# Optimization experiments

Hardware: AMD Instinct MI355X
Metric: run time of the kernel (lower is better)

The kernel has to match this reference:

```python
import jax, jax.numpy as jnp
import numpy as np

H = 32          # num_heads
D = 64          # kv_channels (head dim)
HID = 2048      # hidden_size
MAXPOS = 2048   # max_seq_length


def _rotary_table(num_pos, dim):
    # [num_pos, dim]: sin for first dim/2 cols, cos for last dim/2 cols
    inv_freq = 1.0 / (10000.0 ** (jnp.arange(0, dim, 2, dtype=jnp.float32) / dim))
    t = jnp.arange(num_pos, dtype=jnp.float32)[:, None] * inv_freq[None, :]
    return jnp.concatenate([jnp.sin(t), jnp.cos(t)], axis=1)


def _apply_rope(x, sin, cos):
    # x: [B,S,H,D]; sin,cos: [B,S,D/2]
    sin = jnp.concatenate([sin, sin], axis=-1)[:, :, None, :]  # [B,S,1,D]
    cos = jnp.concatenate([cos, cos], axis=-1)[:, :, None, :]
    half = x.shape[-1] // 2
    x1, x2 = x[..., :half], x[..., half:]
    rot = jnp.concatenate([-x2, x1], axis=-1)
    return x * cos + rot * sin


def setup_inputs() -> dict:
    key = jax.random.key(0)
    k1, k2, k3, k4 = jax.random.split(key, 4)
    B, S = 2, 2048
    hidden_states = jax.random.normal(k1, (B, S, HID), jnp.float32)
    attention_mask = jax.random.randint(k2, (B, 1, S, S), 0, 2).astype(bool)
    position_ids = jnp.broadcast_to(jnp.arange(S, dtype=jnp.int32)[None, :], (B, S))
    W_qkv = jax.random.normal(k3, (3 * H * D, HID), jnp.float32) * 0.02
    W_o = jax.random.normal(k4, (HID, H * D), jnp.float32) * 0.02
    return {"hidden_states": hidden_states, "attention_mask": attention_mask,
            "position_ids": position_ids, "W_qkv": W_qkv, "W_o": W_o}


def reference(hidden_states, attention_mask, position_ids, W_qkv, W_o):
    B, S, _ = hidden_states.shape
    # fused QKV projection (nn.Linear: x @ W.T, no bias)
    qkv = hidden_states @ W_qkv.T                       # [B,S,3*H*D]
    qkv = qkv.reshape(B, S, H, 3 * D)
    q, k, v = jnp.split(qkv, 3, axis=-1)                # each [B,S,H,D]
    sincos = _rotary_table(MAXPOS, D)[position_ids]     # [B,S,D]
    sin, cos = jnp.split(sincos, 2, axis=-1)            # [B,S,D/2] each
    q = _apply_rope(q, sin, cos)
    k = _apply_rope(k, sin, cos)
    scale = jnp.sqrt(jnp.float32(D))
    scores = jnp.einsum('bqhd,bkhd->bhqk', q, k) / scale   # [B,H,S,S]
    scores = jnp.where(attention_mask, jnp.float32(-10000.0), scores)
    weights = jax.nn.softmax(scores, axis=-1)
    attn = jnp.einsum('bhqk,bkhd->bqhd', weights, v)       # [B,S,H,D]
    attn = attn.reshape(B, S, H * D)
    return attn @ W_o.T                                    # [B,S,HID]
```

## Files before the change

kernel.cpp:

```cpp
#include <hip/hip_runtime.h>

#define B_   2
#define S_   2048
#define H_   32
#define D_   64
#define HID_ 2048

typedef unsigned short ushort_t;
typedef __attribute__((ext_vector_type(8))) short short8;
typedef __attribute__((ext_vector_type(4))) float floatx4;

typedef const __attribute__((address_space(1))) char* gas_ptr;
typedef __attribute__((address_space(3))) char* las_ptr;

__device__ __forceinline__ float bf2f(ushort_t u) {
    union { unsigned int i; float f; } v; v.i = ((unsigned int)u) << 16; return v.f;
}
__device__ __forceinline__ ushort_t f2bf(float f) {
    union { float f; unsigned int i; } v; v.f = f;
    unsigned int x = v.i;
    unsigned int r = x + 0x7fffu + ((x >> 16) & 1u);
    return (ushort_t)(r >> 16);
}

__device__ __forceinline__ float fexp2(float x) {
#if __has_builtin(__builtin_amdgcn_exp2f)
    return __builtin_amdgcn_exp2f(x);
#else
    float r; asm("v_exp_f32 %0, %1" : "=v"(r) : "v"(x)); return r;
#endif
}

__device__ __forceinline__ unsigned cvt_pk_bf16(float a, float b) {
    unsigned r;
    asm("v_cvt_pk_bf16_f32 %0, %1, %2" : "=v"(r) : "v"(a), "v"(b));
    return r;
}

__global__ __launch_bounds__(256) void cast_f32_bf16(const float* __restrict__ in,
                                                     ushort_t* __restrict__ out,
                                                     int n8) {
    int i = blockIdx.x * 256 + threadIdx.x;
    if (i >= n8) return;
    const float4* p = (const float4*)(in + (size_t)i * 8);
    float4 a = p[0], b = p[1];
    uint4 o;
    o.x = cvt_pk_bf16(a.x, a.y);
    o.y = cvt_pk_bf16(a.z, a.w);
    o.z = cvt_pk_bf16(b.x, b.y);
    o.w = cvt_pk_bf16(b.z, b.w);
    *(uint4*)(out + (size_t)i * 8) = o;
}

__global__ __launch_bounds__(256) void mask_pack(const int* __restrict__ m,
                                                 unsigned long long* __restrict__ bits) {
    int idx = blockIdx.x * 256 + threadIdx.x;
    unsigned long long bal = __ballot(m[idx] != 0);
    if ((threadIdx.x & 63) == 0) bits[idx >> 6] = bal;
}

__global__ __launch_bounds__(512, 2) void gemm256_bt(const ushort_t* __restrict__ A,
                                                     const ushort_t* __restrict__ Bm,
                                                     ushort_t* __restrict__ C,
                                                     int M, int N, int K) {
    __shared__ ushort_t lA[2][256][64];
    __shared__ ushort_t lB[2][256][64];
    const int tid  = threadIdx.x;
    const int w    = tid >> 6, lane = tid & 63;
    const int quad = lane >> 4, l16 = lane & 15;
    const int wm = w >> 2, wn = w & 3;
    const int sr = lane >> 3, ss = lane & 7;
    const int gseg = (ss ^ sr) * 8;

    const int nbx = N >> 8;
    int id  = blockIdx.x;
    int cpx = gridDim.x >> 3;
    int swz = (id & 7) * cpx + (id >> 3);
    int by = swz / nbx, bx = swz - by * nbx;
    const int m0 = by * 256, n0 = bx * 256;

    int arow[2], brow[2];
    arow[0] = w * 8;                       arow[1] = 128 + w * 8;
    brow[0] = (w >> 2) * 64 + (w & 3) * 8; brow[1] = 128 + brow[0];

    const ushort_t *gAf[2], *gAs[2], *gBf[2], *gBs[2];
#pragma unroll
    for (int c = 0; c < 2; c++) {
        gAf[c] = A  + (size_t)(m0 + arow[c] + sr) * K + gseg;
        gAs[c] = A  + (size_t)(m0 + arow[c] + 64 + sr) * K + gseg;
        gBf[c] = Bm + (size_t)(n0 + brow[c] + sr) * K + gseg;
        gBs[c] = Bm + (size_t)(n0 + brow[c] + 32 + sr) * K + gseg;
    }

#define STAGE_AF(BUF, KT) do { _Pragma("unroll") for (int c = 0; c < 2; c++) \
    __builtin_amdgcn_global_load_lds((gas_ptr)(gAf[c] + (KT)), (las_ptr)&lA[BUF][arow[c]][0], 16, 0, 0); } while (0)
#define STAGE_AS(BUF, KT) do { _Pragma("unroll") for (int c = 0; c < 2; c++) \
    __builtin_amdgcn_global_load_lds((gas_ptr)(gAs[c] + (KT)), (las_ptr)&lA[BUF][arow[c] + 64][0], 16, 0, 0); } while (0)
#define STAGE_BF(BUF, KT) do { _Pragma("unroll") for (int c = 0; c < 2; c++) \
    __builtin_amdgcn_global_load_lds((gas_ptr)(gBf[c] + (KT)), (las_ptr)&lB[BUF][brow[c]][0], 16, 0, 0); } while (0)
#define STAGE_BS(BUF, KT) do { _Pragma("unroll") for (int c = 0; c < 2; c++) \
    __builtin_amdgcn_global_load_lds((gas_ptr)(gBs[c] + (KT)), (las_ptr)&lB[BUF][brow[c] + 32][0], 16, 0, 0); } while (0)

#define LDA_(SUB, BUF) do { _Pragma("unroll") for (int mi = 0; mi < 4; mi++) \
    _Pragma("unroll") for (int ks = 0; ks < 2; ks++) \
        aF[mi][ks] = *(const short8*)&lA[BUF][wm * 128 + (SUB) * 64 + mi * 16 + l16][(((ks * 4 + quad) ^ (l16 & 7)) * 8)]; } while (0)
#define LDB_(SUB, BUF) do { _Pragma("unroll") for (int ni = 0; ni < 2; ni++) \
    _Pragma("unroll") for (int ks = 0; ks < 2; ks++) \
        bF[ni][ks] = *(const short8*)&lB[BUF][wn * 64 + (SUB) * 32 + ni * 16 + l16][(((ks * 4 + quad) ^ (l16 & 7)) * 8)]; } while (0)

#define MM_(Hh, Gg) do { _Pragma("unroll") for (int mi = 0; mi < 4; mi++) \
    _Pragma("unroll") for (int ni = 0; ni < 2; ni++) \
    _Pragma("unroll") for (int ks = 0; ks < 2; ks++) \
        acc[(Hh) * 4 + mi][(Gg) * 2 + ni] = __builtin_amdgcn_mfma_f32_16x16x32_bf16( \
            aF[mi][ks], bF[ni][ks], acc[(Hh) * 4 + mi][(Gg) * 2 + ni], 0, 0, 0); } while (0)

#define VMC6 asm volatile("s_waitcnt vmcnt(6)" ::: "memory")
#define BARR __builtin_amdgcn_s_barrier()
#define SETP1 __builtin_amdgcn_s_setprio(1)
#define SETP0 __builtin_amdgcn_s_setprio(0)

    floatx4 acc[8][4];
#pragma unroll
    for (int i = 0; i < 8; i++)
#pragma unroll
        for (int j = 0; j < 4; j++) acc[i][j] = (floatx4){0.f, 0.f, 0.f, 0.f};
    short8 aF[4][2];
    short8 bF[2][2];

    const int NT = K >> 6;
    const int NI = NT >> 1;

    STAGE_AF(0, 0); STAGE_BF(0, 0); STAGE_AS(0, 0); STAGE_BS(0, 0);
    STAGE_BF(1, 64); STAGE_AS(1, 64); STAGE_BS(1, 64);
    VMC6;
    BARR;

    for (int i = 0; i < NI; ++i) {
        const int t0k = i << 7;
        const int t1k = t0k + 64;
        const int t2k = t0k + 128, t3k = t0k + 192;
        const bool g2 = (t2k < K), g3 = (t3k < K);
        const bool last = (i == NI - 1);

        LDA_(0, 0); LDB_(0, 0);
        STAGE_AF(1, t1k);
        asm volatile("s_waitcnt lgkmcnt(8)" ::: "memory");
        BARR; SETP1; MM_(0, 0); SETP0;
        VMC6; BARR;
        LDA_(1, 0);
        if (g2) STAGE_BF(0, t2k);
        BARR; SETP1; MM_(1, 0); SETP0;
        VMC6; BARR;
        LDB_(1, 0);
        if (g2) STAGE_AS(0, t2k);
        BARR; SETP1; MM_(1, 1); SETP0;
        VMC6; BARR;
        LDA_(0, 0);
        if (g2) STAGE_BS(0, t2k);
        BARR; SETP1; MM_(0, 1); SETP0;
        if (last) { asm volatile("s_waitcnt vmcnt(0)" ::: "memory"); }
        else      { VMC6; }
        BARR;

        LDA_(0, 1); LDB_(0, 1);
        if (g2) STAGE_AF(0, t2k);
        asm volatile("s_waitcnt lgkmcnt(8)" ::: "memory");
        BARR; SETP1; MM_(0, 0); SETP0;
        VMC6; BARR;
        LDA_(1, 1);
        if (g3) STAGE_BF(1, t3k);
        BARR; SETP1; MM_(1, 0); SETP0;
        VMC6; BARR;
        LDB_(1, 1);
        if (g3) STAGE_AS(1, t3k);
        BARR; SETP1; MM_(1, 1); SETP0;
        VMC6; BARR;
        LDA_(0, 1);
        if (g3) STAGE_BS(1, t3k);
        BARR; SETP1; MM_(0, 1); SETP0;
        VMC6; BARR;
    }

#pragma unroll
    for (int mi = 0; mi < 8; mi++)
#pragma unroll
        for (int ni = 0; ni < 4; ni++)
#pragma unroll
            for (int r = 0; r < 4; r++) {
                int row = m0 + wm * 128 + mi * 16 + quad * 4 + r;
                int col = n0 + wn * 64 + ni * 16 + l16;
                C[(size_t)row * N + col] = f2bf(acc[mi][ni][r]);
            }
#undef STAGE_AF
#undef STAGE_AS
#undef STAGE_BF
#undef STAGE_BS
#undef LDA_
#undef LDB_
#undef MM_
#undef VMC6
#undef BARR
#undef SETP1
#undef SETP0
}

template <bool OF32>
__global__ __launch_bounds__(256) void gemm_bt(const ushort_t* __restrict__ A,
                                               const ushort_t* __restrict__ Bm,
                                               void* __restrict__ Cv,
                                               int M, int N, int K) {
    __shared__ ushort_t lA[128 * 32];
    __shared__ ushort_t lB[128 * 32];
    const int tid  = threadIdx.x;
    const int lane = tid & 63, wave = tid >> 6;
    const int quad = lane >> 4, l16 = lane & 15;
    const int wm = wave >> 1, wn = wave & 1;
    const int m0 = blockIdx.y * 128, n0 = blockIdx.x * 128;

    const int srow = tid >> 2;
    const int gseg = (tid & 3) ^ ((tid >> 3) & 3);
    const ushort_t* gA = A + (size_t)(m0 + srow) * K + gseg * 8;
    const ushort_t* gB = Bm + (size_t)(n0 + srow) * K + gseg * 8;

    const int fseg = quad ^ ((l16 >> 1) & 3);

    floatx4 acc[4][4];
#pragma unroll
    for (int i = 0; i < 4; i++)
#pragma unroll
        for (int j = 0; j < 4; j++) acc[i][j] = (floatx4){0.f, 0.f, 0.f, 0.f};

    for (int k0 = 0; k0 < K; k0 += 32) {
#pragma unroll
        for (int j = 0; j < 2; j++) {
            __builtin_amdgcn_global_load_lds(
                (gas_ptr)(gA + (size_t)j * 64 * K + k0),
                (las_ptr)(lA + j * 2048 + wave * 512), 16, 0, 0);
            __builtin_amdgcn_global_load_lds(
                (gas_ptr)(gB + (size_t)j * 64 * K + k0),
                (las_ptr)(lB + j * 2048 + wave * 512), 16, 0, 0);
        }
        __syncthreads();

        short8 aF[4], bF[4];
#pragma unroll
        for (int mi = 0; mi < 4; mi++)
            aF[mi] = *(const short8*)&lA[(wm * 64 + mi * 16 + l16) * 32 + fseg * 8];
#pragma unroll
        for (int ni = 0; ni < 4; ni++)
            bF[ni] = *(const short8*)&lB[(wn * 64 + ni * 16 + l16) * 32 + fseg * 8];
#pragma unroll
        for (int mi = 0; mi < 4; mi++)
#pragma unroll
            for (int ni = 0; ni < 4; ni++)
                acc[mi][ni] = __builtin_amdgcn_mfma_f32_16x16x32_bf16(aF[mi], bF[ni], acc[mi][ni], 0, 0, 0);
        __syncthreads();
    }

#pragma unroll
    for (int mi = 0; mi < 4; mi++)
#pragma unroll
        for (int ni = 0; ni < 4; ni++)
#pragma unroll
            for (int r = 0; r < 4; r++) {
                int row = m0 + wm * 64 + mi * 16 + quad * 4 + r;
                int col = n0 + wn * 64 + ni * 16 + l16;
                if (OF32) ((float*)Cv)[(size_t)row * N + col] = acc[mi][ni][r];
                else      ((ushort_t*)Cv)[(size_t)row * N + col] = f2bf(acc[mi][ni][r]);
            }
}

__global__ __launch_bounds__(256) void rope_qk(const ushort_t* __restrict__ qkv,
                                               const int* __restrict__ pos,
                                               ushort_t* __restrict__ qr,
                                               ushort_t* __restrict__ kr) {
    int idx = blockIdx.x * 256 + threadIdx.x;
    int d = idx & 63;
    int s = (idx >> 6) & 2047;
    int h = (idx >> 17) & 31;
    int b = idx >> 22;
    size_t qbase = ((size_t)(b * S_ + s)) * (3 * H_ * D_) + h * (3 * D_);
    int i  = d & 31;
    int d2 = d ^ 32;
    float x   = bf2f(qkv[qbase + d]);
    float xp  = bf2f(qkv[qbase + d2]);
    float kx  = bf2f(qkv[qbase + 64 + d]);
    float kxp = bf2f(qkv[qbase + 64 + d2]);
    int   p   = pos[b * S_ + s];
    float inv = fexp2((float)i * -0.41524101186092985f);
    float t   = (float)p * inv;
    float c = cosf(t), sn = sinf(t);
    float rq = (d < 32) ? -xp : xp;
    float rk = (d < 32) ? -kxp : kxp;
    float qo = (x * c + rq * sn) * 0.18033688011112042f;
    float ko = kx * c + rk * sn;
    size_t o = ((size_t)(b * H_ + h) * S_ + s) * D_ + d;
    qr[o] = f2bf(qo);
    kr[o] = f2bf(ko);
}

__global__ __launch_bounds__(256) void v_trans(const ushort_t* __restrict__ qkv,
                                               ushort_t* __restrict__ vt) {
    __shared__ ushort_t tile[64][72];
    const int bid = blockIdx.x;
    const int g  = bid >> 5;
    const int s0 = (bid & 31) * 64;
    const int b = g >> 5, h = g & 31;
    const int tid = threadIdx.x;
    const int r = tid >> 2, c = (tid & 3) * 16;
    const ushort_t* src = qkv + ((size_t)(b * S_) + s0 + r) * (3 * H_ * D_) + h * (3 * D_) + 128 + c;
    *(short8*)&tile[r][c]     = *(const short8*)src;
    *(short8*)&tile[r][c + 8] = *(const short8*)(src + 8);
    __syncthreads();
    const int d = tid >> 2, cs = (tid & 3) * 16;
    ushort_t* dst = vt + ((size_t)g * D_ + d) * S_ + s0 + cs;
    short8 o0, o1;
#pragma unroll
    for (int j = 0; j < 8; j++) {
        o0[j] = (short)tile[cs + j][d];
        o1[j] = (short)tile[cs + 8 + j][d];
    }
    *(short8*)dst       = o0;
    *(short8*)(dst + 8) = o1;
}

__global__ __launch_bounds__(256) void attn_kernel(const ushort_t* __restrict__ qr,
                                                   const ushort_t* __restrict__ kr,
                                                   const ushort_t* __restrict__ vt,
                                                   const unsigned long long* __restrict__ mbits,
                                                   ushort_t* __restrict__ ctx) {
    __shared__ ushort_t lK[64 * 64];
    __shared__ ushort_t lV[64 * 64];
    __shared__ ushort_t lds_p[4][16][72];
    const int tid  = threadIdx.x;
    const int wave = tid >> 6, lane = tid & 63;
    const int quad = lane >> 4, l16 = lane & 15;

    const int id   = blockIdx.x;
    const int g    = (id & 7) | ((id >> 8) << 3);
    const int qblk = (id >> 3) & 31;
    const int b    = g >> 5;
    const int q0   = qblk * 64 + wave * 16;
    const size_t headBase = (size_t)g * S_ * D_;
    const unsigned long long* mrow = mbits + ((size_t)b * S_ + q0 + l16) * (S_ / 64);

    const int sr = lane >> 3, ss = lane & 7;
    const int gss = ss ^ sr;
    const ushort_t* gK0 = kr + headBase + (size_t)(wave * 16 + sr) * D_ + gss * 8;
    const ushort_t* gV0 = vt + headBase + (size_t)(wave * 16 + sr) * S_ + gss * 8;

    const int segA0 = ((quad)     ^ (l16 & 7)) * 8;
    const int segA1 = ((quad + 4) ^ (l16 & 7)) * 8;
    const int rowOff = (l16)*64;

    short8 qf0 = *(const short8*)(qr + headBase + (size_t)(q0 + l16) * D_ + quad * 8);
    short8 qf1 = *(const short8*)(qr + headBase + (size_t)(q0 + l16) * D_ + 32 + quad * 8);

    float l_st = 0.f;
    floatx4 o[4];
#pragma unroll
    for (int t = 0; t < 4; t++) o[t] = (floatx4){0.f, 0.f, 0.f, 0.f};

    for (int k0 = 0; k0 < S_; k0 += 64) {
#pragma unroll
        for (int i = 0; i < 2; i++) {
            __builtin_amdgcn_global_load_lds(
                (gas_ptr)(gK0 + (size_t)(k0 + i * 8) * D_),
                (las_ptr)(lK + (wave * 16 + i * 8) * 64), 16, 0, 0);
            __builtin_amdgcn_global_load_lds(
                (gas_ptr)(gV0 + (size_t)(i * 8) * S_ + k0),
                (las_ptr)(lV + (wave * 16 + i * 8) * 64), 16, 0, 0);
        }
        unsigned long long mb = mrow[k0 >> 6];
        __syncthreads();

        floatx4 scT[4];
#pragma unroll
        for (int t = 0; t < 4; t++) scT[t] = (floatx4){0.f, 0.f, 0.f, 0.f};
#pragma unroll
        for (int t = 0; t < 4; t++) {
            short8 kf0 = *(const short8*)&lK[t * 1024 + rowOff + segA0];
            short8 kf1 = *(const short8*)&lK[t * 1024 + rowOff + segA1];
            scT[t] = __builtin_amdgcn_mfma_f32_16x16x32_bf16(kf0, qf0, scT[t], 0, 0, 0);
            scT[t] = __builtin_amdgcn_mfma_f32_16x16x32_bf16(kf1, qf1, scT[t], 0, 0, 0);
        }

        unsigned mlo = (unsigned)(mb >> (quad * 4));
        unsigned mhi = (unsigned)(mb >> (quad * 4 + 32));
        float pv[4][4];
        float rs = 0.f;
#pragma unroll
        for (int t = 0; t < 4; t++) {
            unsigned msrc = (t < 2) ? mlo : mhi;
#pragma unroll
            for (int r = 0; r < 4; r++) {
                int bitpos = (t & 1) * 16 + r;
                float e = fexp2(scT[t][r]);
                e = ((msrc >> bitpos) & 1u) ? 0.f : e;
                pv[t][r] = e;
                rs += e;
            }
        }
        l_st += rs;

#pragma unroll
        for (int t = 0; t < 4; t++) {
            uint2 w;
            w.x = cvt_pk_bf16(pv[t][0], pv[t][1]);
            w.y = cvt_pk_bf16(pv[t][2], pv[t][3]);
            *(uint2*)&lds_p[wave][l16][t * 16 + quad * 4] = w;
        }
        short8 pf0 = *(const short8*)&lds_p[wave][l16][quad * 8];
        short8 pf1 = *(const short8*)&lds_p[wave][l16][32 + quad * 8];

#pragma unroll
        for (int t = 0; t < 4; t++) {
            short8 vf0 = *(const short8*)&lV[t * 1024 + rowOff + segA0];
            short8 vf1 = *(const short8*)&lV[t * 1024 + rowOff + segA1];
            o[t] = __builtin_amdgcn_mfma_f32_16x16x32_bf16(pf0, vf0, o[t], 0, 0, 0);
            o[t] = __builtin_amdgcn_mfma_f32_16x16x32_bf16(pf1, vf1, o[t], 0, 0, 0);
        }
        __syncthreads();
    }

    l_st += __shfl_xor(l_st, 16);
    l_st += __shfl_xor(l_st, 32);
    float li[4];
#pragma unroll
    for (int r = 0; r < 4; r++) li[r] = 1.0f / __shfl(l_st, quad * 4 + r, 16);
#pragma unroll
    for (int t = 0; t < 4; t++)
#pragma unroll
        for (int r = 0; r < 4; r++) {
            int srow = q0 + quad * 4 + r;
            ctx[((size_t)(b * S_) + srow) * (H_ * D_) + (g & 31) * D_ + t * 16 + l16] = f2bf(o[t][r] * li[r]);
        }
}

extern "C" void kernel_launch(void* const* d_in, const int* in_sizes, int n_in,
                              void* d_out, int out_size, void* d_ws, size_t ws_size,
                              hipStream_t stream) {
    const float* hidden          = (const float*)d_in[0];
    const int* mask              = (const int*)d_in[1];
    const int* pos               = (const int*)d_in[2];
    const float* Wqkv            = (const float*)d_in[3];
    const float* Wo              = (const float*)d_in[4];
    float* out                   = (float*)d_out;

    char* ws = (char*)d_ws;
    ushort_t* qkv     = (ushort_t*)(ws);
    ushort_t* ctx     = (ushort_t*)(ws);
    unsigned long long* mbits = (unsigned long long*)(ws + 16777216);
    ushort_t* Wo_bf   = (ushort_t*)(ws + 50331648);
    ushort_t* hid_bf  = (ushort_t*)(ws + 58720256);
    ushort_t* Wqkv_bf = (ushort_t*)(ws + 75497472);
    ushort_t* q_r     = (ushort_t*)(ws + 58720256);
    ushort_t* k_r     = (ushort_t*)(ws + 75497472);
    ushort_t* v_t     = (ushort_t*)(ws + 92274688);

    {
        int n8 = (B_ * S_ * HID_) / 8;
        cast_f32_bf16<<<n8 / 256, 256, 0, stream>>>(hidden, hid_bf, n8);
        n8 = (3 * H_ * D_ * HID_) / 8;
        cast_f32_bf16<<<n8 / 256, 256, 0, stream>>>(Wqkv, Wqkv_bf, n8);
        n8 = (HID_ * H_ * D_) / 8;
        cast_f32_bf16<<<n8 / 256, 256, 0, stream>>>(Wo, Wo_bf, n8);
    }

    gemm256_bt<<<((3 * H_ * D_) / 256) * ((B_ * S_) / 256), 512, 0, stream>>>(
        hid_bf, Wqkv_bf, qkv, B_ * S_, 3 * H_ * D_, HID_);

    int nElem = B_ * H_ * S_ * D_;
    rope_qk<<<nElem / 256, 256, 0, stream>>>(qkv, pos, q_r, k_r);
    v_trans<<<B_ * H_ * (S_ / 64), 256, 0, stream>>>(qkv, v_t);

    mask_pack<<<(B_ * S_ * S_) / 256, 256, 0, stream>>>(mask, mbits);

    attn_kernel<<<2048, 256, 0, stream>>>(q_r, k_r, v_t, mbits, ctx);

    gemm_bt<true><<<dim3(HID_ / 128, (B_ * S_) / 128), 256, 0, stream>>>(
        ctx, Wo_bf, out, B_ * S_, HID_, H_ * D_);
}
```

Measured before the change: 363.2 us.

## Restructure 256x256 GEMM main loop into per-tile ping-pong with double B fragments

Rewrites the big GEMM's K-loop from a two-tile unrolled schedule into a per-64-K-tile loop with a two-iteration epilogue. It double-buffers the B register fragments (bF0/bF1) and reorders the MMA quadrants so that each LDS fragment load is issued right after an MFMA block, with sched_barrier fences keeping the compiler from moving them. The aim is to overlap LDS reads and global-to-LDS staging with MFMA work and to drop the per-iteration guard branches. In exchange it uses more VGPRs and relies on a hand-tuned vmcnt wait sequence in the tail, which could cause races or register spills if any count is wrong.

```diff
diff --git a/kernel.cpp b/kernel.cpp
--- a/kernel.cpp
+++ b/kernel.cpp
@@ -104,20 +104,24 @@
 #define LDA_(SUB, BUF) do { _Pragma("unroll") for (int mi = 0; mi < 4; mi++) \
     _Pragma("unroll") for (int ks = 0; ks < 2; ks++) \
         aF[mi][ks] = *(const short8*)&lA[BUF][wm * 128 + (SUB) * 64 + mi * 16 + l16][(((ks * 4 + quad) ^ (l16 & 7)) * 8)]; } while (0)
-#define LDB_(SUB, BUF) do { _Pragma("unroll") for (int ni = 0; ni < 2; ni++) \
+#define LDB_(SUB, BUF, BV) do { _Pragma("unroll") for (int ni = 0; ni < 2; ni++) \
     _Pragma("unroll") for (int ks = 0; ks < 2; ks++) \
-        bF[ni][ks] = *(const short8*)&lB[BUF][wn * 64 + (SUB) * 32 + ni * 16 + l16][(((ks * 4 + quad) ^ (l16 & 7)) * 8)]; } while (0)
-
-#define MM_(Hh, Gg) do { _Pragma("unroll") for (int mi = 0; mi < 4; mi++) \
+        BV[ni][ks] = *(const short8*)&lB[BUF][wn * 64 + (SUB) * 32 + ni * 16 + l16][(((ks * 4 + quad) ^ (l16 & 7)) * 8)]; } while (0)
+
+#define MM_(Hh, Gg, BV) do { _Pragma("unroll") for (int mi = 0; mi < 4; mi++) \
     _Pragma("unroll") for (int ni = 0; ni < 2; ni++) \
     _Pragma("unroll") for (int ks = 0; ks < 2; ks++) \
         acc[(Hh) * 4 + mi][(Gg) * 2 + ni] = __builtin_amdgcn_mfma_f32_16x16x32_bf16( \
-            aF[mi][ks], bF[ni][ks], acc[(Hh) * 4 + mi][(Gg) * 2 + ni], 0, 0, 0); } while (0)
+            aF[mi][ks], BV[ni][ks], acc[(Hh) * 4 + mi][(Gg) * 2 + ni], 0, 0, 0); } while (0)
 
 #define VMC6 asm volatile("s_waitcnt vmcnt(6)" ::: "memory")
+#define VMC4 asm volatile("s_waitcnt vmcnt(4)" ::: "memory")
+#define VMC2 asm volatile("s_waitcnt vmcnt(2)" ::: "memory")
+#define VMC0 asm volatile("s_waitcnt vmcnt(0)" ::: "memory")
 #define BARR __builtin_amdgcn_s_barrier()
 #define SETP1 __builtin_amdgcn_s_setprio(1)
 #define SETP0 __builtin_amdgcn_s_setprio(0)
+#define SCHED0 __builtin_amdgcn_sched_barrier(0)
 
     floatx4 acc[8][4];
 #pragma unroll
@@ -125,60 +129,84 @@
 #pragma unroll
         for (int j = 0; j < 4; j++) acc[i][j] = (floatx4){0.f, 0.f, 0.f, 0.f};
     short8 aF[4][2];
-    short8 bF[2][2];
+    short8 bF0[2][2];
+    short8 bF1[2][2];
 
     const int NT = K >> 6;
-    const int NI = NT >> 1;
-
-    STAGE_AF(0, 0); STAGE_BF(0, 0); STAGE_AS(0, 0); STAGE_BS(0, 0);
-    STAGE_BF(1, 64); STAGE_AS(1, 64); STAGE_BS(1, 64);
+
+    STAGE_AF(0, 0); STAGE_BF(0, 0); STAGE_BS(0, 0); STAGE_AS(0, 0);
+    STAGE_AF(1, 64); STAGE_BF(1, 64);
     VMC6;
     BARR;
-
-    for (int i = 0; i < NI; ++i) {
-        const int t0k = i << 7;
-        const int t1k = t0k + 64;
-        const int t2k = t0k + 128, t3k = t0k + 192;
-        const bool g2 = (t2k < K), g3 = (t3k < K);
-        const bool last = (i == NI - 1);
-
-        LDA_(0, 0); LDB_(0, 0);
-        STAGE_AF(1, t1k);
-        asm volatile("s_waitcnt lgkmcnt(8)" ::: "memory");
-        BARR; SETP1; MM_(0, 0); SETP0;
+    LDA_(0, 0);
+    LDB_(0, 0, bF0);
+
+    for (int t = 0; t < NT - 2; ++t) {
+        const int buf = t & 1, nb = buf ^ 1;
+        const int kt1 = (t + 1) << 6, kt2 = (t + 2) << 6;
+
+        STAGE_BS(nb, kt1);
+        BARR; SETP1; MM_(0, 0, bF0); SETP0;
+        SCHED0;
+        LDB_(1, buf, bF1);
         VMC6; BARR;
-        LDA_(1, 0);
-        if (g2) STAGE_BF(0, t2k);
-        BARR; SETP1; MM_(1, 0); SETP0;
+
+        STAGE_AS(nb, kt1);
+        BARR; SETP1; MM_(0, 1, bF1); SETP0;
+        SCHED0;
+        LDA_(1, buf);
         VMC6; BARR;
-        LDB_(1, 0);
-        if (g2) STAGE_AS(0, t2k);
-        BARR; SETP1; MM_(1, 1); SETP0;
+
+        STAGE_AF(buf, kt2);
+        BARR; SETP1; MM_(1, 1, bF1); SETP0;
         VMC6; BARR;
-        LDA_(0, 0);
-        if (g2) STAGE_BS(0, t2k);
-        BARR; SETP1; MM_(0, 1); SETP0;
-        if (last) { asm volatile("s_waitcnt vmcnt(0)" ::: "memory"); }
-        else      { VMC6; }
+
+        STAGE_BF(buf, kt2);
+        BARR; SETP1; MM_(1, 0, bF0); SETP0;
+        SCHED0;
+        LDA_(0, nb);
+        LDB_(0, nb, bF0);
+        VMC6; BARR;
+    }
+
+    {
+        const int t = NT - 2;
+        const int buf = t & 1, nb = buf ^ 1;
+        const int kt1 = (t + 1) << 6;
+
+        STAGE_BS(nb, kt1);
+        BARR; SETP1; MM_(0, 0, bF0); SETP0;
+        SCHED0; LDB_(1, buf, bF1);
+        VMC6; BARR;
+
+        STAGE_AS(nb, kt1);
+        BARR; SETP1; MM_(0, 1, bF1); SETP0;
+        SCHED0; LDA_(1, buf);
+        VMC6; BARR;
+
+        BARR; SETP1; MM_(1, 1, bF1); SETP0;
+        VMC4; BARR;
+
+        BARR; SETP1; MM_(1, 0, bF0); SETP0;
+        SCHED0; LDA_(0, nb); LDB_(0, nb, bF0);
+        VMC2; BARR;
+    }
+
+    {
+        const int buf = (NT - 1) & 1;
+
+        BARR; SETP1; MM_(0, 0, bF0); SETP0;
+        SCHED0; LDB_(1, buf, bF1);
+        VMC0; BARR;
+
+        BARR; SETP1; MM_(0, 1, bF1); SETP0;
+        SCHED0; LDA_(1, buf);
         BARR;
 
-        LDA_(0, 1); LDB_(0, 1);
-        if (g2) STAGE_AF(0, t2k);
-        asm volatile("s_waitcnt lgkmcnt(8)" ::: "memory");
-        BARR; SETP1; MM_(0, 0); SETP0;
-        VMC6; BARR;
-        LDA_(1, 1);
-        if (g3) STAGE_BF(1, t3k);
-        BARR; SETP1; MM_(1, 0); SETP0;
-        VMC6; BARR;
-        LDB_(1, 1);
-        if (g3) STAGE_AS(1, t3k);
-        BARR; SETP1; MM_(1, 1); SETP0;
-        VMC6; BARR;
-        LDA_(0, 1);
-        if (g3) STAGE_BS(1, t3k);
-        BARR; SETP1; MM_(0, 1); SETP0;
-        VMC6; BARR;
+        BARR; SETP1; MM_(1, 1, bF1); SETP0;
+        BARR;
+
+        BARR; SETP1; MM_(1, 0, bF0); SETP0;
     }
 
 #pragma unroll
@@ -199,9 +227,13 @@
 #undef LDB_
 #undef MM_
 #undef VMC6
+#undef VMC4
+#undef VMC2
+#undef VMC0
 #undef BARR
 #undef SETP1
 #undef SETP0
+#undef SCHED0
 }
 
 template <bool OF32>
```

Measured after the change: 365.4 us. About the same (+0.6%).

## Prefetch next K/V tile in attention and widen output-projection GEMM tiles

Applied to the files above, without the earlier changes.

The attention loop now loads all K and V fragments from LDS into registers right after the barrier, syncs, and then issues the global-to-LDS copy for the next tile. That copy overlaps with the QK^T, softmax and PV compute instead of being exposed at the start of every iteration. The output projection GEMM moves to 512-thread blocks with 128x256 tiles and grouped block-index swizzling, which improves operand reuse and L2 locality. In exchange, register pressure rises because the kf/vf arrays are held across the compute, and the wider GEMM launches fewer blocks.

```diff
diff --git a/kernel.cpp b/kernel.cpp
--- a/kernel.cpp
+++ b/kernel.cpp
@@ -136,9 +136,8 @@
     BARR;
 
     for (int i = 0; i < NI; ++i) {
-        const int t0k = i << 7;
-        const int t1k = t0k + 64;
-        const int t2k = t0k + 128, t3k = t0k + 192;
+        const int t1k = (i << 7) + 64;
+        const int t2k = t1k + 64, t3k = t1k + 128;
         const bool g2 = (t2k < K), g3 = (t3k < K);
         const bool last = (i == NI - 1);
 
@@ -205,24 +204,32 @@
 }
 
 template <bool OF32>
-__global__ __launch_bounds__(256) void gemm_bt(const ushort_t* __restrict__ A,
-                                               const ushort_t* __restrict__ Bm,
-                                               void* __restrict__ Cv,
-                                               int M, int N, int K) {
-    __shared__ ushort_t lA[128 * 32];
-    __shared__ ushort_t lB[128 * 32];
+__global__ __launch_bounds__(512, 4) void gemm_wide_bt(const ushort_t* __restrict__ A,
+                                                       const ushort_t* __restrict__ Bm,
+                                                       void* __restrict__ Cv,
+                                                       int M, int N, int K) {
+    __shared__ ushort_t lA[128][32];
+    __shared__ ushort_t lB[256][32];
     const int tid  = threadIdx.x;
-    const int lane = tid & 63, wave = tid >> 6;
+    const int w    = tid >> 6, lane = tid & 63;
     const int quad = lane >> 4, l16 = lane & 15;
-    const int wm = wave >> 1, wn = wave & 1;
-    const int m0 = blockIdx.y * 128, n0 = blockIdx.x * 128;
-
-    const int srow = tid >> 2;
-    const int gseg = (tid & 3) ^ ((tid >> 3) & 3);
-    const ushort_t* gA = A + (size_t)(m0 + srow) * K + gseg * 8;
-    const ushort_t* gB = Bm + (size_t)(n0 + srow) * K + gseg * 8;
-
-    const int fseg = quad ^ ((l16 >> 1) & 3);
+    const int wm = w >> 2, wn = w & 3;
+
+    const int sr = lane >> 2, ss = lane & 3;
+    const int gss = ss ^ ((sr >> 1) & 3);
+
+    const int nbx = N >> 8;
+    int id  = blockIdx.x;
+    int cpx = gridDim.x >> 3;
+    int swz = (id & 7) * cpx + (id >> 3);
+    int by = swz / nbx, bx = swz - by * nbx;
+    const int m0 = by * 128, n0 = bx * 256;
+
+    const ushort_t* gA  = A  + (size_t)(m0 + w * 16 + sr) * K + gss * 8;
+    const ushort_t* gB0 = Bm + (size_t)(n0 + w * 32 + sr) * K + gss * 8;
+    const ushort_t* gB1 = gB0 + (size_t)16 * K;
+
+    const int fseg = (quad ^ ((l16 >> 1) & 3)) * 8;
 
     floatx4 acc[4][4];
 #pragma unroll
@@ -231,24 +238,21 @@
         for (int j = 0; j < 4; j++) acc[i][j] = (floatx4){0.f, 0.f, 0.f, 0.f};
 
     for (int k0 = 0; k0 < K; k0 += 32) {
-#pragma unroll
-        for (int j = 0; j < 2; j++) {
-            __builtin_amdgcn_global_load_lds(
-                (gas_ptr)(gA + (size_t)j * 64 * K + k0),
-                (las_ptr)(lA + j * 2048 + wave * 512), 16, 0, 0);
-            __builtin_amdgcn_global_load_lds(
-                (gas_ptr)(gB + (size_t)j * 64 * K + k0),
-                (las_ptr)(lB + j * 2048 + wave * 512), 16, 0, 0);
-        }
+        __builtin_amdgcn_global_load_lds((gas_ptr)(gA + k0),
+                                         (las_ptr)&lA[w * 16][0], 16, 0, 0);
+        __builtin_amdgcn_global_load_lds((gas_ptr)(gB0 + k0),
+                                         (las_ptr)&lB[w * 32][0], 16, 0, 0);
+        __builtin_amdgcn_global_load_lds((gas_ptr)(gB1 + k0),
+                                         (las_ptr)&lB[w * 32 + 16][0], 16, 0, 0);
         __syncthreads();
 
         short8 aF[4], bF[4];
 #pragma unroll
         for (int mi = 0; mi < 4; mi++)
-            aF[mi] = *(const short8*)&lA[(wm * 64 + mi * 16 + l16) * 32 + fseg * 8];
+            aF[mi] = *(const short8*)&lA[wm * 64 + mi * 16 + l16][fseg];
 #pragma unroll
         for (int ni = 0; ni < 4; ni++)
-            bF[ni] = *(const short8*)&lB[(wn * 64 + ni * 16 + l16) * 32 + fseg * 8];
+            bF[ni] = *(const short8*)&lB[wn * 64 + ni * 16 + l16][fseg];
 #pragma unroll
         for (int mi = 0; mi < 4; mi++)
 #pragma unroll
@@ -353,6 +357,12 @@
     const int segA1 = ((quad + 4) ^ (l16 & 7)) * 8;
     const int rowOff = (l16)*64;
 
+#define STAGE_T(K0) do { _Pragma("unroll") for (int i = 0; i < 2; i++) { \
+    __builtin_amdgcn_global_load_lds((gas_ptr)(gK0 + (size_t)((K0) + i * 8) * D_), \
+                                     (las_ptr)(lK + (wave * 16 + i * 8) * 64), 16, 0, 0); \
+    __builtin_amdgcn_global_load_lds((gas_ptr)(gV0 + (size_t)(i * 8) * S_ + (K0)), \
+                                     (las_ptr)(lV + (wave * 16 + i * 8) * 64), 16, 0, 0); } } while (0)
+
     short8 qf0 = *(const short8*)(qr + headBase + (size_t)(q0 + l16) * D_ + quad * 8);
     short8 qf1 = *(const short8*)(qr + headBase + (size_t)(q0 + l16) * D_ + 32 + quad * 8);
 
@@ -361,28 +371,31 @@
 #pragma unroll
     for (int t = 0; t < 4; t++) o[t] = (floatx4){0.f, 0.f, 0.f, 0.f};
 
+    STAGE_T(0);
+
     for (int k0 = 0; k0 < S_; k0 += 64) {
-#pragma unroll
-        for (int i = 0; i < 2; i++) {
-            __builtin_amdgcn_global_load_lds(
-                (gas_ptr)(gK0 + (size_t)(k0 + i * 8) * D_),
-                (las_ptr)(lK + (wave * 16 + i * 8) * 64), 16, 0, 0);
-            __builtin_amdgcn_global_load_lds(
-                (gas_ptr)(gV0 + (size_t)(i * 8) * S_ + k0),
-                (las_ptr)(lV + (wave * 16 + i * 8) * 64), 16, 0, 0);
-        }
         unsigned long long mb = mrow[k0 >> 6];
         __syncthreads();
 
+        short8 kf[4][2], vf[4][2];
+#pragma unroll
+        for (int t = 0; t < 4; t++) {
+            kf[t][0] = *(const short8*)&lK[t * 1024 + rowOff + segA0];
+            kf[t][1] = *(const short8*)&lK[t * 1024 + rowOff + segA1];
+            vf[t][0] = *(const short8*)&lV[t * 1024 + rowOff + segA0];
+            vf[t][1] = *(const short8*)&lV[t * 1024 + rowOff + segA1];
+        }
+        __syncthreads();
+
+        if (k0 + 64 < S_) STAGE_T(k0 + 64);
+
         floatx4 scT[4];
 #pragma unroll
         for (int t = 0; t < 4; t++) scT[t] = (floatx4){0.f, 0.f, 0.f, 0.f};
 #pragma unroll
         for (int t = 0; t < 4; t++) {
-            short8 kf0 = *(const short8*)&lK[t * 1024 + rowOff + segA0];
-            short8 kf1 = *(const short8*)&lK[t * 1024 + rowOff + segA1];
-            scT[t] = __builtin_amdgcn_mfma_f32_16x16x32_bf16(kf0, qf0, scT[t], 0, 0, 0);
-            scT[t] = __builtin_amdgcn_mfma_f32_16x16x32_bf16(kf1, qf1, scT[t], 0, 0, 0);
+            scT[t] = __builtin_amdgcn_mfma_f32_16x16x32_bf16(kf[t][0], qf0, scT[t], 0, 0, 0);
+            scT[t] = __builtin_amdgcn_mfma_f32_16x16x32_bf16(kf[t][1], qf1, scT[t], 0, 0, 0);
         }
 
         unsigned mlo = (unsigned)(mb >> (quad * 4));
@@ -415,13 +428,11 @@
 
 #pragma unroll
         for (int t = 0; t < 4; t++) {
-            short8 vf0 = *(const short8*)&lV[t * 1024 + rowOff + segA0];
-            short8 vf1 = *(const short8*)&lV[t * 1024 + rowOff + segA1];
-            o[t] = __builtin_amdgcn_mfma_f32_16x16x32_bf16(pf0, vf0, o[t], 0, 0, 0);
-            o[t] = __builtin_amdgcn_mfma_f32_16x16x32_bf16(pf1, vf1, o[t], 0, 0, 0);
-        }
-        __syncthreads();
-    }
+            o[t] = __builtin_amdgcn_mfma_f32_16x16x32_bf16(pf0, vf[t][0], o[t], 0, 0, 0);
+            o[t] = __builtin_amdgcn_mfma_f32_16x16x32_bf16(pf1, vf[t][1], o[t], 0, 0, 0);
+        }
+    }
+#undef STAGE_T
 
     l_st += __shfl_xor(l_st, 16);
     l_st += __shfl_xor(l_st, 32);
@@ -478,6 +489,6 @@
 
     attn_kernel<<<2048, 256, 0, stream>>>(q_r, k_r, v_t, mbits, ctx);
 
-    gemm_bt<true><<<dim3(HID_ / 128, (B_ * S_) / 128), 256, 0, stream>>>(
+    gemm_wide_bt<true><<<(HID_ / 256) * ((B_ * S_) / 128), 512, 0, stream>>>(
         ctx, Wo_bf, out, B_ * S_, HID_, H_ * D_);
 }
```

Measured after the change: 370.1 us. About the same (+1.9%).
